# Kernel tuning notes

Hardware: AMD Instinct MI355X
Metric: run time of the kernel (lower is better)

## Reference

```python
import jax, jax.numpy as jnp
import numpy as np

E = 11        # number of language experts
ALPHA = 1000.0  # soft-argmax temperature
C1 = 8.0      # gate sharpness


def setup_inputs() -> dict:
    key = jax.random.key(0)
    ks = jax.random.split(key, 6)
    B, S, H, L = 16, 256, 1024, 32
    return {
        "transformer_out": jax.random.normal(ks[0], (B, S, H), dtype=jnp.float32),
        "logits_ld": jax.random.normal(ks[1], (B, E), dtype=jnp.float32),
        "W1": jax.random.normal(ks[2], (E, H, H), dtype=jnp.float32) * 0.02,
        "b1": jax.random.normal(ks[3], (E, H), dtype=jnp.float32) * 0.02,
        "W2": jax.random.normal(ks[4], (E, H, L), dtype=jnp.float32) * 0.02,
        "b2": jax.random.normal(ks[5], (E, L), dtype=jnp.float32) * 0.02,
    }


def reference(transformer_out, logits_ld, W1, b1, W2, b2):
    # soft argmax over language-detect logits -> continuous lang id per sample [B]
    sm = jax.nn.softmax(logits_ld * ALPHA, axis=1)
    lang_id = jnp.sum(sm * jnp.arange(logits_ld.shape[1], dtype=logits_ld.dtype), axis=1)

    # soft top-hat gate per expert i: sigmoid((id-(i-.5))*c1)*sigmoid(((i+.5)-id)*c1) -> [E,B]
    idx = jnp.arange(E, dtype=lang_id.dtype)[:, None]          # [E,1]
    gate = (jax.nn.sigmoid((lang_id[None, :] - (idx - 0.5)) * C1)
            * jax.nn.sigmoid((idx + 0.5 - lang_id[None, :]) * C1))  # [E,B]

    # all 11 expert FFN branches as batched GEMMs (dropout = identity in eval)
    h = jax.nn.relu(jnp.einsum('bsh,ehd->ebsd', transformer_out, W1)
                    + b1[:, None, None, :])                     # [E,B,S,H]
    t = jnp.einsum('ebsd,edl->ebsl', h, W2) + b2[:, None, None, :]  # [E,B,S,L]

    # gate per (expert, batch) and sum over experts -> [B,S,L]
    logits = jnp.einsum('ebsl,eb->bsl', t, gate)
    return logits
```

## Files before the change

### kernel.cpp

```cpp
#include <hip/hip_runtime.h>
#include <hip/hip_bf16.h>
#include <stdint.h>

#define E_ 11
#define B_ 16
#define S_ 256
#define H_ 1024
#define L_ 32
#define GEPS 1e-4f

typedef __attribute__((ext_vector_type(8))) short short8;
typedef __attribute__((ext_vector_type(4))) float f32x4;

__device__ __forceinline__ unsigned short f2bf(float f) {
  unsigned u = __float_as_uint(f);
  unsigned r = (u + 0x7FFFu + ((u >> 16) & 1u)) >> 16;
  return (unsigned short)r;
}
__device__ __forceinline__ float bf2f(unsigned short v) {
  return __uint_as_float(((unsigned)v) << 16);
}
__device__ __forceinline__ void gload_lds16(const void* g, void* l) {
  __builtin_amdgcn_global_load_lds(
      (const __attribute__((address_space(1))) unsigned int*)g,
      (__attribute__((address_space(3))) unsigned int*)l, 16, 0, 0);
}
__device__ __forceinline__ float sigf(float x) { return 1.0f / (1.0f + expf(-x)); }

__device__ __forceinline__ float lang_of(const float* __restrict__ logits, int b) {
  float lv[E_];
  float m = -1e30f;
  #pragma unroll
  for (int i = 0; i < E_; ++i) { lv[i] = logits[b * E_ + i]; m = fmaxf(m, lv[i]); }
  float den = 0.f, num = 0.f;
  #pragma unroll
  for (int i = 0; i < E_; ++i) {
    float z = expf((lv[i] - m) * 1000.0f);
    den += z; num += z * (float)i;
  }
  return num / den;
}
__device__ __forceinline__ float gate_of(float lang, int e) {
  float fe = (float)e;
  return sigf((lang - (fe - 0.5f)) * 8.0f) * sigf(((fe + 0.5f) - lang) * 8.0f);
}

__device__ __forceinline__ bool expert_active(const float* __restrict__ logits, int e) {
  int b = threadIdx.x & 15;
  float lang = lang_of(logits, b);
  unsigned long long m = __ballot(fabsf(lang - (float)e) < 1.7f);
  return m != 0ull;
}

__global__ __launch_bounds__(256) void prep_kernel(
    const float* __restrict__ x, const float* __restrict__ logits,
    const float* __restrict__ W1, const float* __restrict__ W2,
    unsigned short* __restrict__ xbf, unsigned short* __restrict__ W1T,
    unsigned short* __restrict__ W2T, int* __restrict__ plan) {
  int bid = blockIdx.x;
  int tid = threadIdx.x;
  __shared__ float t[64][65];

  if (bid < 2048) {
    int i = (bid * 256 + tid) * 8;
    float4 f0 = *(const float4*)(x + i);
    float4 f1 = *(const float4*)(x + i + 4);
    short8 o;
    o[0] = (short)f2bf(f0.x); o[1] = (short)f2bf(f0.y);
    o[2] = (short)f2bf(f0.z); o[3] = (short)f2bf(f0.w);
    o[4] = (short)f2bf(f1.x); o[5] = (short)f2bf(f1.y);
    o[6] = (short)f2bf(f1.z); o[7] = (short)f2bf(f1.w);
    *(short8*)(xbf + i) = o;
    return;
  }
  if (bid < 2048 + 2816) {
    int tt = bid - 2048;
    int e = tt >> 8, rest = tt & 255;
    int k0 = (rest >> 4) * 64, d0 = (rest & 15) * 64;
    if (!expert_active(logits, e)) return;
    int kr = tid >> 2, dc = (tid & 3) * 16;
    const float* src = W1 + ((size_t)e << 20) + (size_t)(k0 + kr) * H_ + d0 + dc;
    #pragma unroll
    for (int q = 0; q < 4; ++q) {
      float4 v = *(const float4*)(src + q * 4);
      t[kr][dc + q * 4 + 0] = v.x; t[kr][dc + q * 4 + 1] = v.y;
      t[kr][dc + q * 4 + 2] = v.z; t[kr][dc + q * 4 + 3] = v.w;
    }
    __syncthreads();
    int dr = tid >> 2, kc = (tid & 3) * 16;
    short8 v0, v1;
    #pragma unroll
    for (int j = 0; j < 8; ++j) v0[j] = (short)f2bf(t[kc + j][dr]);
    #pragma unroll
    for (int j = 0; j < 8; ++j) v1[j] = (short)f2bf(t[kc + 8 + j][dr]);
    unsigned short* dst = W1T + ((size_t)e << 20) + (size_t)(d0 + dr) * H_ + k0 + kc;
    *(short8*)(dst) = v0;
    *(short8*)(dst + 8) = v1;
    return;
  }
  if (bid < 2048 + 2816 + 176) {
    int tt = bid - 4864;
    int e = tt >> 4, k0 = (tt & 15) * 64;
    if (!expert_active(logits, e)) return;
    int kr = tid >> 2, lc = (tid & 3) * 8;
    const float* src = W2 + (size_t)e * H_ * L_ + (size_t)(k0 + kr) * L_ + lc;
    float4 a = *(const float4*)(src);
    float4 b = *(const float4*)(src + 4);
    t[kr][lc + 0] = a.x; t[kr][lc + 1] = a.y; t[kr][lc + 2] = a.z; t[kr][lc + 3] = a.w;
    t[kr][lc + 4] = b.x; t[kr][lc + 5] = b.y; t[kr][lc + 6] = b.z; t[kr][lc + 7] = b.w;
    __syncthreads();
    int lr = tid >> 3, kc = (tid & 7) * 8;
    short8 v;
    #pragma unroll
    for (int j = 0; j < 8; ++j) v[j] = (short)f2bf(t[kc + j][lr]);
    *(short8*)(W2T + (size_t)(e * L_ + lr) * H_ + k0 + kc) = v;
    return;
  }
  {
    __shared__ float langs[16];
    __shared__ int wcnt[4];
    if (tid < 16) langs[tid] = lang_of(logits, tid);
    __syncthreads();
    bool act = false;
    if (tid < E_ * B_) {
      int e = tid >> 4, b = tid & 15;
      act = gate_of(langs[b], e) >= GEPS;
    }
    unsigned long long m = __ballot(act);
    int w = tid >> 6;
    if ((tid & 63) == 0) wcnt[w] = __popcll(m);
    __syncthreads();
    int off = 0;
    for (int i = 0; i < w; ++i) off += wcnt[i];
    int rank = __popcll(m & ((1ull << (tid & 63)) - 1ull));
    if (act) plan[1 + off + rank] = tid;
    if (tid == 0) plan[0] = wcnt[0] + wcnt[1] + wcnt[2] + wcnt[3];
  }
}

#define WAITV(N) asm volatile("s_waitcnt vmcnt(" #N ")" ::: "memory")

__global__ __launch_bounds__(512, 2) void ffn_kernel(
    const unsigned short* __restrict__ xbf, const unsigned short* __restrict__ W1T,
    const unsigned short* __restrict__ W2T, const float* __restrict__ b1,
    const float* __restrict__ b2, const float* __restrict__ logits,
    const int* __restrict__ plan, float* __restrict__ out) {
  int bid = blockIdx.x;
  int cnt = plan[0];
  if (bid >= (cnt << 2)) return;
  int pair = plan[1 + (bid >> 2)];
  int dt = bid & 3;
  int e = pair >> 4, b = pair & 15;
  float g = gate_of(lang_of(logits, b), e);

  __shared__ __align__(16) char smem[98304];

  int tid = threadIdx.x;
  int w = tid >> 6, wr = w >> 1, wc = w & 1;
  int l = tid & 63, l15 = l & 15, l4 = l >> 4;

  const unsigned short* gA[2]; int ldsA[2];
  const unsigned short* gB[2]; int ldsB[2];
  #pragma unroll
  for (int jj = 0; jj < 2; ++jj) {
    int c = jj * 512 + tid;
    int p = c >> 3, uu = (c & 7) ^ (p & 7);
    int row = p * 2 + (uu >> 2), kc = (uu & 3) * 8;
    gA[jj] = xbf + (size_t)(b * S_ + row) * H_ + kc;
    ldsA[jj] = c * 16;
    gB[jj] = W1T + ((size_t)e * H_ + dt * 256 + row) * H_ + kc;
    ldsB[jj] = 16384 + c * 16;
  }
  int offA[4], offB[8];
  #pragma unroll
  for (int mf = 0; mf < 4; ++mf) {
    int row = wr * 64 + mf * 16 + l15;
    int p = row >> 1;
    int slot = (((row & 1) * 4) + l4) ^ (p & 7);
    offA[mf] = p * 128 + slot * 16;
  }
  #pragma unroll
  for (int nf = 0; nf < 8; ++nf) {
    int d = wc * 128 + nf * 16 + l15;
    int p = d >> 1;
    int slot = (((d & 1) * 4) + l4) ^ (p & 7);
    offB[nf] = 16384 + p * 128 + slot * 16;
  }

  f32x4 acc[4][8];
  #pragma unroll
  for (int mf = 0; mf < 4; ++mf)
    #pragma unroll
    for (int nf = 0; nf < 8; ++nf) acc[mf][nf] = f32x4{0.f, 0.f, 0.f, 0.f};

  auto stage = [&](int buf, int kt) {
    int bb = buf * 32768;
    int ko = kt * 32;
    gload_lds16(gA[0] + ko, smem + bb + ldsA[0]);
    gload_lds16(gA[1] + ko, smem + bb + ldsA[1]);
    gload_lds16(gB[0] + ko, smem + bb + ldsB[0]);
    gload_lds16(gB[1] + ko, smem + bb + ldsB[1]);
  };

  stage(0, 0);
  stage(1, 1);

  #pragma unroll
  for (int kt = 0; kt < 32; ++kt) {
    __builtin_amdgcn_s_barrier();
    if (kt < 30) {
      stage((kt + 2) % 3, kt + 2);
      WAITV(8);
    } else if (kt == 30) {
      WAITV(4);
    } else {
      WAITV(0);
    }
    __builtin_amdgcn_s_barrier();
    int bb = (kt % 3) * 32768;
    short8 af[4], bf[8];
    #pragma unroll
    for (int mf = 0; mf < 4; ++mf) af[mf] = *(const short8*)(smem + bb + offA[mf]);
    #pragma unroll
    for (int nf = 0; nf < 8; ++nf) bf[nf] = *(const short8*)(smem + bb + offB[nf]);
    asm volatile("s_waitcnt lgkmcnt(0)" ::: "memory");
    __builtin_amdgcn_sched_barrier(0);
    __builtin_amdgcn_s_setprio(1);
    #pragma unroll
    for (int mf = 0; mf < 4; ++mf)
      #pragma unroll
      for (int nf = 0; nf < 8; ++nf)
        acc[mf][nf] =
            __builtin_amdgcn_mfma_f32_16x16x32_bf16(af[mf], bf[nf], acc[mf][nf], 0, 0, 0);
    __builtin_amdgcn_s_setprio(0);
  }

  __syncthreads();

  float b1v[8];
  #pragma unroll
  for (int nf = 0; nf < 8; ++nf)
    b1v[nf] = b1[e * H_ + dt * 256 + wc * 128 + nf * 16 + l15];

  char* P = smem + w * 8192;
  f32x4 tacc[4][2];
  #pragma unroll
  for (int mf = 0; mf < 4; ++mf)
    #pragma unroll
    for (int nl = 0; nl < 2; ++nl) tacc[mf][nl] = f32x4{0.f, 0.f, 0.f, 0.f};

  #pragma unroll
  for (int half = 0; half < 2; ++half) {
    #pragma unroll
    for (int mf = 0; mf < 4; ++mf)
      #pragma unroll
      for (int nfh = 0; nfh < 4; ++nfh) {
        int nf = half * 4 + nfh;
        #pragma unroll
        for (int rr = 0; rr < 4; ++rr) {
          int row = mf * 16 + l4 * 4 + rr;
          int col = nfh * 16 + l15;
          float v = fmaxf(acc[mf][nf][rr] + b1v[nf], 0.f);
          *(unsigned short*)(P + row * 128 + (((col >> 3) ^ (row & 7)) * 16) +
                             (col & 7) * 2) = f2bf(v);
        }
      }
    asm volatile("s_waitcnt lgkmcnt(0)" ::: "memory");
    #pragma unroll
    for (int kk = 0; kk < 2; ++kk) {
      short8 ap[4], bw[2];
      #pragma unroll
      for (int mf = 0; mf < 4; ++mf) {
        int row = mf * 16 + l15;
        int ch = kk * 4 + l4;
        ap[mf] = *(const short8*)(P + row * 128 + ((ch ^ (row & 7)) * 16));
      }
      #pragma unroll
      for (int nl = 0; nl < 2; ++nl)
        bw[nl] = *(const short8*)(W2T + (size_t)(e * L_ + nl * 16 + l15) * H_ +
                                  dt * 256 + wc * 128 + half * 64 + kk * 32 + l4 * 8);
      #pragma unroll
      for (int mf = 0; mf < 4; ++mf)
        #pragma unroll
        for (int nl = 0; nl < 2; ++nl)
          tacc[mf][nl] =
              __builtin_amdgcn_mfma_f32_16x16x32_bf16(ap[mf], bw[nl], tacc[mf][nl], 0, 0, 0);
    }
    asm volatile("s_waitcnt lgkmcnt(0)" ::: "memory");
  }

  float* Tr = (float*)smem + w * 2048;
  #pragma unroll
  for (int mf = 0; mf < 4; ++mf)
    #pragma unroll
    for (int nl = 0; nl < 2; ++nl)
      #pragma unroll
      for (int rr = 0; rr < 4; ++rr) {
        int row = mf * 16 + l4 * 4 + rr;
        int col = nl * 16 + l15;
        Tr[row * 32 + col] = tacc[mf][nl][rr];
      }
  __syncthreads();
  float* Tb = (float*)smem;
  #pragma unroll
  for (int jj = 0; jj < 16; ++jj) {
    int ei = tid + jj * 512;
    int srow = ei >> 5, lcol = ei & 31;
    int wr2 = srow >> 6, r6 = srow & 63;
    float sum = Tb[(wr2 * 2 + 0) * 2048 + r6 * 32 + lcol] +
                Tb[(wr2 * 2 + 1) * 2048 + r6 * 32 + lcol];
    if (dt == 0) sum += b2[e * L_ + lcol];
    atomicAdd(out + (size_t)(b * S_ + srow) * L_ + lcol, g * sum);
  }
}

__global__ void fb_kernel(const float* __restrict__ x, const float* __restrict__ logits,
                          const float* __restrict__ W1, const float* __restrict__ b1,
                          const float* __restrict__ W2, const float* __restrict__ b2,
                          float* __restrict__ out) {
  int bid = blockIdx.x;
  int e = bid >> 9;
  int r = bid & 511;
  int b = r >> 5, st = r & 31, s0 = st * 8;
  float g = gate_of(lang_of(logits, b), e);
  if (g < GEPS) return;

  __shared__ float xs[8][H_];
  __shared__ unsigned short hs[8][H_];
  int tid = threadIdx.x;
  for (int jj = 0; jj < 32; ++jj) {
    int idx = tid + jj * 256;
    int s = idx >> 10, k = idx & 1023;
    xs[s][k] = x[(size_t)(b * S_ + s0 + s) * H_ + k];
  }
  __syncthreads();
  for (int qq = 0; qq < 4; ++qq) {
    int d = tid + qq * 256;
    float a[8];
    #pragma unroll
    for (int s = 0; s < 8; ++s) a[s] = 0.f;
    for (int k = 0; k < H_; ++k) {
      float wv = W1[((size_t)e << 20) + (size_t)k * H_ + d];
      #pragma unroll
      for (int s = 0; s < 8; ++s) a[s] += xs[s][k] * wv;
    }
    float bv = b1[e * H_ + d];
    #pragma unroll
    for (int s = 0; s < 8; ++s) hs[s][d] = f2bf(fmaxf(a[s] + bv, 0.f));
  }
  __syncthreads();
  int s = tid >> 5, lcol = tid & 31;
  float acc = 0.f;
  for (int d = 0; d < H_; ++d)
    acc += bf2f(hs[s][d]) * W2[(size_t)(e * H_ + d) * L_ + lcol];
  acc += b2[e * L_ + lcol];
  atomicAdd(out + (size_t)(b * S_ + s0 + s) * L_ + lcol, g * acc);
}

extern "C" void kernel_launch(void* const* d_in, const int* in_sizes, int n_in,
                              void* d_out, int out_size, void* d_ws, size_t ws_size,
                              hipStream_t stream) {
  (void)in_sizes; (void)n_in;
  const float* x  = (const float*)d_in[0];
  const float* lg = (const float*)d_in[1];
  const float* W1 = (const float*)d_in[2];
  const float* b1 = (const float*)d_in[3];
  const float* W2 = (const float*)d_in[4];
  const float* b2 = (const float*)d_in[5];
  float* out = (float*)d_out;

  hipMemsetAsync(d_out, 0, (size_t)out_size * sizeof(float), stream);

  const size_t OFF_X = 0;
  const size_t OFF_W1 = OFF_X + 8388608;
  const size_t OFF_W2 = OFF_W1 + 23068672;
  const size_t OFF_PLAN = OFF_W2 + 720896;
  const size_t WS_NEED = OFF_PLAN + 1024;

  if (ws_size >= WS_NEED) {
    unsigned short* xbf = (unsigned short*)((char*)d_ws + OFF_X);
    unsigned short* W1T = (unsigned short*)((char*)d_ws + OFF_W1);
    unsigned short* W2T = (unsigned short*)((char*)d_ws + OFF_W2);
    int* plan = (int*)((char*)d_ws + OFF_PLAN);
    prep_kernel<<<2048 + 2816 + 176 + 1, 256, 0, stream>>>(x, lg, W1, W2, xbf, W1T, W2T, plan);
    ffn_kernel<<<704, 512, 0, stream>>>(xbf, W1T, W2T, b1, b2, lg, plan, out);
  } else {
    fb_kernel<<<E_ * B_ * (S_ / 8), 256, 0, stream>>>(x, lg, W1, b1, W2, b2, out);
  }
}
```

Baseline: 65.09 us.

## Pre-swizzle activations into MFMA fragment order and load A directly to registers

The prep kernel now writes the bf16 activations in a tiled layout that matches the MFMA A-fragment order. The FFN kernel loads A fragments straight from global memory into registers, double-buffered one k-step ahead, and no longer stages them through LDS. This cuts LDS traffic and LDS footprint per k-step, since only W1T tiles are staged, and halves the shared buffer stride. In exchange it adds register pressure and exposes global-load latency on A, and duplicate reads by the two column waves now rely on the cache.

```diff
diff --git a/kernel.cpp b/kernel.cpp
--- a/kernel.cpp
+++ b/kernel.cpp
@@ -55,7 +55,7 @@
 __global__ __launch_bounds__(256) void prep_kernel(
     const float* __restrict__ x, const float* __restrict__ logits,
     const float* __restrict__ W1, const float* __restrict__ W2,
-    unsigned short* __restrict__ xbf, unsigned short* __restrict__ W1T,
+    unsigned short* __restrict__ xbfS, unsigned short* __restrict__ W1T,
     unsigned short* __restrict__ W2T, int* __restrict__ plan) {
   int bid = blockIdx.x;
   int tid = threadIdx.x;
@@ -70,7 +70,11 @@
     o[2] = (short)f2bf(f0.z); o[3] = (short)f2bf(f0.w);
     o[4] = (short)f2bf(f1.x); o[5] = (short)f2bf(f1.y);
     o[6] = (short)f2bf(f1.z); o[7] = (short)f2bf(f1.w);
-    *(short8*)(xbf + i) = o;
+    int k = i & 1023, s = (i >> 10) & 255, b = i >> 18;
+    int tile = b * 4 + (s >> 6), srow = s & 63;
+    size_t chunk = ((((size_t)tile * 32 + (k >> 5)) * 4 + (srow >> 4)) * 16 + (srow & 15)) * 4
+                   + ((k >> 3) & 3);
+    *(short8*)(xbfS + chunk * 8) = o;
     return;
   }
   if (bid < 2048 + 2816) {
@@ -141,7 +145,7 @@
 #define WAITV(N) asm volatile("s_waitcnt vmcnt(" #N ")" ::: "memory")
 
 __global__ __launch_bounds__(512, 2) void ffn_kernel(
-    const unsigned short* __restrict__ xbf, const unsigned short* __restrict__ W1T,
+    const unsigned short* __restrict__ xbfS, const unsigned short* __restrict__ W1T,
     const unsigned short* __restrict__ W2T, const float* __restrict__ b1,
     const float* __restrict__ b2, const float* __restrict__ logits,
     const int* __restrict__ plan, float* __restrict__ out) {
@@ -158,33 +162,29 @@
   int tid = threadIdx.x;
   int w = tid >> 6, wr = w >> 1, wc = w & 1;
   int l = tid & 63, l15 = l & 15, l4 = l >> 4;
-
-  const unsigned short* gA[2]; int ldsA[2];
+  int lane8 = (l15 * 4 + l4) * 8;
+
+  const unsigned short* pA[4];
+  #pragma unroll
+  for (int mf = 0; mf < 4; ++mf)
+    pA[mf] = xbfS + (size_t)((b * 4 + wr) * 128 + mf) * 512 + lane8;
+
   const unsigned short* gB[2]; int ldsB[2];
   #pragma unroll
   for (int jj = 0; jj < 2; ++jj) {
     int c = jj * 512 + tid;
     int p = c >> 3, uu = (c & 7) ^ (p & 7);
     int row = p * 2 + (uu >> 2), kc = (uu & 3) * 8;
-    gA[jj] = xbf + (size_t)(b * S_ + row) * H_ + kc;
-    ldsA[jj] = c * 16;
     gB[jj] = W1T + ((size_t)e * H_ + dt * 256 + row) * H_ + kc;
-    ldsB[jj] = 16384 + c * 16;
-  }
-  int offA[4], offB[8];
-  #pragma unroll
-  for (int mf = 0; mf < 4; ++mf) {
-    int row = wr * 64 + mf * 16 + l15;
-    int p = row >> 1;
-    int slot = (((row & 1) * 4) + l4) ^ (p & 7);
-    offA[mf] = p * 128 + slot * 16;
-  }
+    ldsB[jj] = c * 16;
+  }
+  int offB[8];
   #pragma unroll
   for (int nf = 0; nf < 8; ++nf) {
     int d = wc * 128 + nf * 16 + l15;
     int p = d >> 1;
     int slot = (((d & 1) * 4) + l4) ^ (p & 7);
-    offB[nf] = 16384 + p * 128 + slot * 16;
+    offB[nf] = p * 128 + slot * 16;
   }
 
   f32x4 acc[4][8];
@@ -193,34 +193,32 @@
     #pragma unroll
     for (int nf = 0; nf < 8; ++nf) acc[mf][nf] = f32x4{0.f, 0.f, 0.f, 0.f};
 
-  auto stage = [&](int buf, int kt) {
-    int bb = buf * 32768;
+  auto stageB = [&](int buf, int kt) {
+    int bb = buf * 16384;
     int ko = kt * 32;
-    gload_lds16(gA[0] + ko, smem + bb + ldsA[0]);
-    gload_lds16(gA[1] + ko, smem + bb + ldsA[1]);
     gload_lds16(gB[0] + ko, smem + bb + ldsB[0]);
     gload_lds16(gB[1] + ko, smem + bb + ldsB[1]);
   };
-
-  stage(0, 0);
-  stage(1, 1);
-
-  #pragma unroll
-  for (int kt = 0; kt < 32; ++kt) {
+  auto prefA = [&](short8 (&dst)[4], int kt) {
+    #pragma unroll
+    for (int mf = 0; mf < 4; ++mf) dst[mf] = *(const short8*)(pA[mf] + kt * 2048);
+  };
+
+  short8 fA0[4], fA1[4];
+  stageB(0, 0);
+  stageB(1, 1);
+  prefA(fA0, 0);
+
+  auto KSTEP = [&](short8 (&cur)[4], short8 (&nxt)[4], int kt) {
     __builtin_amdgcn_s_barrier();
-    if (kt < 30) {
-      stage((kt + 2) % 3, kt + 2);
-      WAITV(8);
-    } else if (kt == 30) {
-      WAITV(4);
-    } else {
-      WAITV(0);
-    }
+    if (kt < 30) stageB((kt + 2) % 3, kt + 2);
+    if (kt < 31) prefA(nxt, kt + 1);
+    if (kt < 30) { WAITV(12); }
+    else if (kt == 30) { WAITV(10); }
+    else { WAITV(4); }
     __builtin_amdgcn_s_barrier();
-    int bb = (kt % 3) * 32768;
-    short8 af[4], bf[8];
-    #pragma unroll
-    for (int mf = 0; mf < 4; ++mf) af[mf] = *(const short8*)(smem + bb + offA[mf]);
+    int bb = (kt % 3) * 16384;
+    short8 bf[8];
     #pragma unroll
     for (int nf = 0; nf < 8; ++nf) bf[nf] = *(const short8*)(smem + bb + offB[nf]);
     asm volatile("s_waitcnt lgkmcnt(0)" ::: "memory");
@@ -231,8 +229,14 @@
       #pragma unroll
       for (int nf = 0; nf < 8; ++nf)
         acc[mf][nf] =
-            __builtin_amdgcn_mfma_f32_16x16x32_bf16(af[mf], bf[nf], acc[mf][nf], 0, 0, 0);
+            __builtin_amdgcn_mfma_f32_16x16x32_bf16(cur[mf], bf[nf], acc[mf][nf], 0, 0, 0);
     __builtin_amdgcn_s_setprio(0);
+  };
+
+  #pragma unroll 1
+  for (int kt = 0; kt < 32; kt += 2) {
+    KSTEP(fA0, fA1, kt);
+    KSTEP(fA1, fA0, kt + 1);
   }
 
   __syncthreads();
@@ -378,12 +382,12 @@
   const size_t WS_NEED = OFF_PLAN + 1024;
 
   if (ws_size >= WS_NEED) {
-    unsigned short* xbf = (unsigned short*)((char*)d_ws + OFF_X);
+    unsigned short* xbfS = (unsigned short*)((char*)d_ws + OFF_X);
     unsigned short* W1T = (unsigned short*)((char*)d_ws + OFF_W1);
     unsigned short* W2T = (unsigned short*)((char*)d_ws + OFF_W2);
     int* plan = (int*)((char*)d_ws + OFF_PLAN);
-    prep_kernel<<<2048 + 2816 + 176 + 1, 256, 0, stream>>>(x, lg, W1, W2, xbf, W1T, W2T, plan);
-    ffn_kernel<<<704, 512, 0, stream>>>(xbf, W1T, W2T, b1, b2, lg, plan, out);
+    prep_kernel<<<2048 + 2816 + 176 + 1, 256, 0, stream>>>(x, lg, W1, W2, xbfS, W1T, W2T, plan);
+    ffn_kernel<<<704, 512, 0, stream>>>(xbfS, W1T, W2T, b1, b2, lg, plan, out);
   } else {
     fb_kernel<<<E_ * B_ * (S_ / 8), 256, 0, stream>>>(x, lg, W1, b1, W2, b2, out);
   }
```

Result: slower. 74.92 us (+15.1%).
